# Kernel optimization log

Hardware: AMD Instinct MI355X
Metric: run time of the kernel (lower is better)

Reference implementation:

```python
import jax, jax.numpy as jnp
import numpy as np

D_MODEL = 1024
D_STATE = 16
DT_RANK = 64  # d_model // 16 ('auto')
DT_MIN = 0.001
DT_MAX = 0.1


def setup_inputs() -> dict:
    key = jax.random.key(0)
    ks = jax.random.split(key, 7)
    B, S = 2, 2048
    return {
        "x": jax.random.normal(ks[0], (B, S, D_MODEL), jnp.float32),
        "w_in": jax.random.normal(ks[1], (D_MODEL, D_MODEL), jnp.float32) / np.sqrt(D_MODEL).astype(np.float32),
        "w_x": jax.random.normal(ks[2], (D_MODEL, DT_RANK + 2 * D_STATE), jnp.float32) / np.sqrt(D_MODEL).astype(np.float32),
        "w_dt": jax.random.normal(ks[3], (DT_RANK, D_MODEL), jnp.float32) / np.sqrt(DT_RANK).astype(np.float32),
        "b_dt": jnp.zeros((D_MODEL,), jnp.float32),
        "A_log": jax.random.normal(ks[5], (D_MODEL, D_STATE), jnp.float32) * 0.5,
        "Dp": jax.random.normal(ks[6], (D_MODEL,), jnp.float32),
    }


def reference(x, w_in, w_x, w_dt, b_dt, A_log, Dp):
    # x: (b, s, d)
    x_in = jnp.einsum('bsd,de->bse', x, w_in)          # in_proj, (b,s,d_inner=d)
    proj = jnp.einsum('bsd,dp->bsp', x_in, w_x)        # x_proj, (b,s,dt_rank+2n)
    dt_low, Bm, Cm = jnp.split(proj, [DT_RANK, DT_RANK + D_STATE], axis=-1)
    # dt_proj + softplus + range scaling -> (b,s,d)
    dt = jax.nn.softplus(jnp.einsum('bsr,rd->bsd', dt_low, w_dt) + b_dt) * (DT_MAX - DT_MIN) + DT_MIN
    A = -jnp.exp(A_log)                                # (d, n), strictly negative

    b, s, d = x.shape
    h0 = jnp.zeros((b, d, D_STATE), x.dtype)

    # time-major streams for scan
    dt_tm = jnp.swapaxes(dt, 0, 1)     # (s,b,d)
    u_tm = jnp.swapaxes(x_in, 0, 1)    # (s,b,d)
    B_tm = jnp.swapaxes(Bm, 0, 1)      # (s,b,n)
    C_tm = jnp.swapaxes(Cm, 0, 1)      # (s,b,n)

    def step(h, inp):
        dtt, ut, bt, ct = inp
        dA = dtt[:, :, None] * A                      # (b,d,n) = dt[b,d]*A[d,n]
        barA = jnp.exp(dA)
        # bar_B = dA; source sums the input term over channel dim d (keepdim)
        inp_term = jnp.einsum('bdn,bn,bd->bn', dA, bt, ut)  # (b,n)
        h = barA * h + inp_term[:, None, :]           # broadcast over d
        y = jnp.einsum('bdn,bn->bd', h, ct) + Dp * ut # (b,d)
        return h, y

    _, ys = jax.lax.scan(step, h0, (dt_tm, u_tm, B_tm, C_tm))  # ys: (s,b,d)
    return jnp.swapaxes(ys, 0, 1)                     # (b,s,d)
```

## Files before the change

kernel.cpp:

```cpp
#include <hip/hip_runtime.h>
#include <hip/hip_bf16.h>

#define D_MODEL 1024
#define D_STATE 16
#define DT_RANK 64
#define SEQ 2048
#define BATCH 2
#define M_TOTAL 4096
#define CHUNKS 64
#define CLEN 32
#define LOG2E 1.44269504088896f

typedef __bf16 bf16x8 __attribute__((ext_vector_type(8)));
typedef float f32x4 __attribute__((ext_vector_type(4)));

__device__ __forceinline__ unsigned short f2bf(float f) {
    union { float f; unsigned int u; } v; v.f = f;
    unsigned int r = v.u + 0x7FFFu + ((v.u >> 16) & 1u);
    return (unsigned short)(r >> 16);
}
__device__ __forceinline__ float bf2f(unsigned short u) {
    union { unsigned int i; float f; } v; v.i = ((unsigned int)u) << 16; return v.f;
}
__device__ __forceinline__ void gload16(const void* g, void* l) {
    __builtin_amdgcn_global_load_lds(
        (const __attribute__((address_space(1))) unsigned int*)g,
        (__attribute__((address_space(3))) unsigned int*)l, 16, 0, 0);
}
__device__ __forceinline__ float fexp2(float x) { return __builtin_amdgcn_exp2f(x); }

__global__ void __launch_bounds__(256) k_setup(const float* __restrict__ x,
                                               const float* __restrict__ win,
                                               const float* __restrict__ wx,
                                               const float* __restrict__ wdt,
                                               const float* __restrict__ alog,
                                               unsigned short* __restrict__ xb,
                                               unsigned short* __restrict__ bt,
                                               unsigned short* __restrict__ wxT,
                                               unsigned short* __restrict__ wxBC,
                                               unsigned short* __restrict__ wdtT,
                                               float* __restrict__ aneg,
                                               unsigned short* __restrict__ anegT) {
    __shared__ float tile[32][33];
    int blk = blockIdx.x;
    int t = threadIdx.x;
    if (blk < 4096) {
        int i = blk * 256 + t;
        float4 v = reinterpret_cast<const float4*>(x)[i];
        ushort4 o;
        o.x = f2bf(v.x); o.y = f2bf(v.y); o.z = f2bf(v.z); o.w = f2bf(v.w);
        reinterpret_cast<ushort4*>(xb)[i] = o;
    } else if (blk < 5120) {
        int blk2 = blk - 4096;
        int bx = blk2 & 31, by = blk2 >> 5;
        int tx = t & 31, ty = t >> 5;
        int xc = bx * 32 + tx;
#pragma unroll
        for (int j = 0; j < 4; j++)
            tile[ty + 8 * j][tx] = win[(by * 32 + ty + 8 * j) * D_MODEL + xc];
        __syncthreads();
        int x2 = by * 32 + tx;
#pragma unroll
        for (int j = 0; j < 4; j++)
            bt[(bx * 32 + ty + 8 * j) * D_MODEL + x2] = f2bf(tile[tx][ty + 8 * j]);
    } else if (blk < 5376) {
        int idx = (blk - 5120) * 256 + t;
        int e = idx & 1023, p = idx >> 10;
        wxT[p * D_MODEL + e] = f2bf(wx[e * 96 + p]);
    } else if (blk < 5504) {
        int idx = (blk - 5376) * 256 + t;
        int e = idx & 1023, p = idx >> 10;
        wxBC[p * D_MODEL + e] = f2bf(wx[e * 96 + 64 + p]);
    } else if (blk < 5568) {
        int i = (blk - 5504) * 256 + t;
        float v = -expf(alog[i]);
        aneg[i] = v * LOG2E;
        anegT[(i & 15) * D_MODEL + (i >> 4)] = f2bf(v);
    } else {
        int idx = (blk - 5568) * 256 + t;
        int d = idx & 1023, k = idx >> 10;
        wdtT[d * DT_RANK + k] = f2bf(wdt[k * D_MODEL + d]);
    }
}

__global__ void __launch_bounds__(256) k_gemm_xin(const unsigned short* __restrict__ xb,
                                                  const unsigned short* __restrict__ bt,
                                                  unsigned short* __restrict__ xinb) {
    __shared__ unsigned short sA[2][64 * 64];
    __shared__ unsigned short sB[2][128 * 64];
    int bid = blockIdx.x;
    int m0 = (bid & 63) * 64;
    int n0 = (bid >> 6) * 128;
    int t = threadIdx.x;
    int lane = t & 63;
    int w = t >> 6;
    int wm = (w >> 1) * 32, wn = (w & 1) * 64;
    int c = lane & 15, q = lane >> 4;

    const unsigned short* gA[2];
    const unsigned short* gB[4];
#pragma unroll
    for (int L = 0; L < 2; L++) {
        int s = L * 256 + t;
        int row = s >> 3, ch = (s & 7) ^ (row & 7);
        gA[L] = xb + (m0 + row) * D_MODEL + ch * 8;
    }
#pragma unroll
    for (int L = 0; L < 4; L++) {
        int s = L * 256 + t;
        int row = s >> 3, ch = (s & 7) ^ (row & 7);
        gB[L] = bt + (n0 + row) * D_MODEL + ch * 8;
    }

    f32x4 acc[2][4] = {};
    {
        char* la = (char*)&sA[0][0] + w * 1024;
        char* lb = (char*)&sB[0][0] + w * 1024;
#pragma unroll
        for (int L = 0; L < 2; L++) gload16(gA[L], la + L * 4096);
#pragma unroll
        for (int L = 0; L < 4; L++) gload16(gB[L], lb + L * 4096);
    }
    int cur = 0;
    for (int it = 0; it < 16; it++) {
        __syncthreads();
        if (it + 1 < 16) {
            int kn = (it + 1) * 64;
            char* la = (char*)&sA[cur ^ 1][0] + w * 1024;
            char* lb = (char*)&sB[cur ^ 1][0] + w * 1024;
#pragma unroll
            for (int L = 0; L < 2; L++) gload16(gA[L] + kn, la + L * 4096);
#pragma unroll
            for (int L = 0; L < 4; L++) gload16(gB[L] + kn, lb + L * 4096);
        }
#pragma unroll
        for (int kk = 0; kk < 2; kk++) {
            int perm = (((kk << 2) | q) ^ (c & 7)) << 3;
            bf16x8 af[2], bfr[4];
#pragma unroll
            for (int i = 0; i < 2; i++)
                af[i] = *reinterpret_cast<const bf16x8*>(&sA[cur][(wm + i * 16 + c) * 64 + perm]);
#pragma unroll
            for (int j = 0; j < 4; j++)
                bfr[j] = *reinterpret_cast<const bf16x8*>(&sB[cur][(wn + j * 16 + c) * 64 + perm]);
#pragma unroll
            for (int i = 0; i < 2; i++)
#pragma unroll
                for (int j = 0; j < 4; j++)
                    acc[i][j] = __builtin_amdgcn_mfma_f32_16x16x32_bf16(bfr[j], af[i], acc[i][j], 0, 0, 0);
        }
        cur ^= 1;
    }
#pragma unroll
    for (int i = 0; i < 2; i++) {
        int row = m0 + wm + i * 16 + c;
#pragma unroll
        for (int j = 0; j < 4; j++) {
            int col = n0 + wn + j * 16 + q * 4;
            ushort4 o;
            o.x = f2bf(acc[i][j][0]); o.y = f2bf(acc[i][j][1]);
            o.z = f2bf(acc[i][j][2]); o.w = f2bf(acc[i][j][3]);
            *reinterpret_cast<ushort4*>(&xinb[row * D_MODEL + col]) = o;
        }
    }
}

__global__ void __launch_bounds__(256) k_xlow(const unsigned short* __restrict__ xinb,
                                              const unsigned short* __restrict__ wxT,
                                              unsigned short* __restrict__ xlow) {
    int m0 = blockIdx.x * 64;
    int t = threadIdx.x;
    int lane = t & 63, w = t >> 6;
    int c = lane & 15, q = lane >> 4;
    int row = m0 + w * 16 + c;
    f32x4 acc[4] = {};
    const unsigned short* pa = xinb + row * D_MODEL + q * 8;
    const unsigned short* pw = wxT + c * D_MODEL + q * 8;
#pragma unroll 4
    for (int k0 = 0; k0 < D_MODEL; k0 += 32) {
        bf16x8 a0 = *reinterpret_cast<const bf16x8*>(pa + k0);
#pragma unroll
        for (int j = 0; j < 4; j++) {
            bf16x8 wf = *reinterpret_cast<const bf16x8*>(pw + j * 16 * D_MODEL + k0);
            acc[j] = __builtin_amdgcn_mfma_f32_16x16x32_bf16(wf, a0, acc[j], 0, 0, 0);
        }
    }
#pragma unroll
    for (int j = 0; j < 4; j++) {
        ushort4 o;
        o.x = f2bf(acc[j][0]); o.y = f2bf(acc[j][1]);
        o.z = f2bf(acc[j][2]); o.w = f2bf(acc[j][3]);
        *reinterpret_cast<ushort4*>(&xlow[row * DT_RANK + j * 16 + q * 4]) = o;
    }
}

__global__ void __launch_bounds__(256) k_gemm_dt(const unsigned short* __restrict__ xlow,
                                                 const unsigned short* __restrict__ wdtT,
                                                 const float* __restrict__ bdt,
                                                 unsigned short* __restrict__ dtb) {
    __shared__ unsigned short sA[128 * 64];
    int bid = blockIdx.x;
    int m0 = (bid & 31) * 128;
    int n0 = (bid >> 5) * 128;
    int t = threadIdx.x;
    int lane = t & 63, w = t >> 6;
    int c = lane & 15, q = lane >> 4;

    {
        char* la = (char*)&sA[0] + w * 1024;
#pragma unroll
        for (int L = 0; L < 4; L++) {
            int s = L * 256 + t;
            int row = s >> 3, ch = (s & 7) ^ (row & 7);
            gload16(xlow + (m0 + row) * DT_RANK + ch * 8, la + L * 4096);
        }
    }
    __syncthreads();

    int mw = m0 + w * 32;
    f32x4 acc[2][8] = {};
#pragma unroll
    for (int kk = 0; kk < 2; kk++) {
        bf16x8 af[2];
#pragma unroll
        for (int i = 0; i < 2; i++)
            af[i] = *reinterpret_cast<const bf16x8*>(
                &sA[(w * 32 + i * 16 + c) * 64 + ((((kk << 2) | q)) ^ (c & 7)) * 8]);
#pragma unroll
        for (int j = 0; j < 8; j++) {
            bf16x8 bfr = *reinterpret_cast<const bf16x8*>(
                &wdtT[(n0 + j * 16 + c) * DT_RANK + kk * 32 + q * 8]);
            acc[0][j] = __builtin_amdgcn_mfma_f32_16x16x32_bf16(bfr, af[0], acc[0][j], 0, 0, 0);
            acc[1][j] = __builtin_amdgcn_mfma_f32_16x16x32_bf16(bfr, af[1], acc[1][j], 0, 0, 0);
        }
    }
#pragma unroll
    for (int i = 0; i < 2; i++) {
        int row = mw + i * 16 + c;
#pragma unroll
        for (int j = 0; j < 8; j++) {
            int dcol = n0 + j * 16 + q * 4;
            float4 bv = *reinterpret_cast<const float4*>(&bdt[dcol]);
            ushort4 o;
            {
                float xv = acc[i][j][0] + bv.x;
                float sp = fmaxf(xv, 0.f) + __logf(1.f + __expf(-fabsf(xv)));
                o.x = f2bf(sp * 0.099f + 0.001f);
            }
            {
                float xv = acc[i][j][1] + bv.y;
                float sp = fmaxf(xv, 0.f) + __logf(1.f + __expf(-fabsf(xv)));
                o.y = f2bf(sp * 0.099f + 0.001f);
            }
            {
                float xv = acc[i][j][2] + bv.z;
                float sp = fmaxf(xv, 0.f) + __logf(1.f + __expf(-fabsf(xv)));
                o.z = f2bf(sp * 0.099f + 0.001f);
            }
            {
                float xv = acc[i][j][3] + bv.w;
                float sp = fmaxf(xv, 0.f) + __logf(1.f + __expf(-fabsf(xv)));
                o.w = f2bf(sp * 0.099f + 0.001f);
            }
            *reinterpret_cast<ushort4*>(&dtb[row * D_MODEL + dcol]) = o;
        }
    }
}

__global__ void __launch_bounds__(256) k_bcw(const unsigned short* __restrict__ xinb,
                                             const unsigned short* __restrict__ dtb,
                                             const unsigned short* __restrict__ wxBC,
                                             const unsigned short* __restrict__ anegT,
                                             float* __restrict__ bcp,
                                             float* __restrict__ wpp) {
    int bid = blockIdx.x;
    int m0 = (bid & 31) * 128;
    int ks = bid >> 5;
    int kbase = ks * 128;
    int t = threadIdx.x;
    int lane = t & 63, w = t >> 6;
    int c = lane & 15, q = lane >> 4;
    int mw = m0 + w * 32;
    f32x4 accb[2][2] = {};
    f32x4 accw[2] = {};
    const unsigned short* pa0 = xinb + (mw + c) * D_MODEL + kbase + q * 8;
    const unsigned short* pa1 = pa0 + 16 * D_MODEL;
    const unsigned short* pt0 = dtb + (mw + c) * D_MODEL + kbase + q * 8;
    const unsigned short* pt1 = pt0 + 16 * D_MODEL;
    const unsigned short* pb0 = wxBC + c * D_MODEL + kbase + q * 8;
    const unsigned short* pb1 = pb0 + 16 * D_MODEL;
    const unsigned short* pA = anegT + c * D_MODEL + kbase + q * 8;
#pragma unroll
    for (int k0 = 0; k0 < 128; k0 += 32) {
        bf16x8 a0 = *reinterpret_cast<const bf16x8*>(pa0 + k0);
        bf16x8 a1 = *reinterpret_cast<const bf16x8*>(pa1 + k0);
        bf16x8 t0 = *reinterpret_cast<const bf16x8*>(pt0 + k0);
        bf16x8 t1 = *reinterpret_cast<const bf16x8*>(pt1 + k0);
        bf16x8 b0 = *reinterpret_cast<const bf16x8*>(pb0 + k0);
        bf16x8 b1 = *reinterpret_cast<const bf16x8*>(pb1 + k0);
        bf16x8 bA = *reinterpret_cast<const bf16x8*>(pA + k0);
        bf16x8 g0, g1;
#pragma unroll
        for (int e = 0; e < 8; e++) {
            g0[e] = (__bf16)((float)t0[e] * (float)a0[e]);
            g1[e] = (__bf16)((float)t1[e] * (float)a1[e]);
        }
        accb[0][0] = __builtin_amdgcn_mfma_f32_16x16x32_bf16(b0, a0, accb[0][0], 0, 0, 0);
        accb[0][1] = __builtin_amdgcn_mfma_f32_16x16x32_bf16(b1, a0, accb[0][1], 0, 0, 0);
        accb[1][0] = __builtin_amdgcn_mfma_f32_16x16x32_bf16(b0, a1, accb[1][0], 0, 0, 0);
        accb[1][1] = __builtin_amdgcn_mfma_f32_16x16x32_bf16(b1, a1, accb[1][1], 0, 0, 0);
        accw[0] = __builtin_amdgcn_mfma_f32_16x16x32_bf16(bA, g0, accw[0], 0, 0, 0);
        accw[1] = __builtin_amdgcn_mfma_f32_16x16x32_bf16(bA, g1, accw[1], 0, 0, 0);
    }
#pragma unroll
    for (int i = 0; i < 2; i++) {
        int row = mw + i * 16 + c;
#pragma unroll
        for (int j = 0; j < 2; j++)
            *reinterpret_cast<f32x4*>(&bcp[(ks * M_TOTAL + row) * 32 + j * 16 + q * 4]) = accb[i][j];
        *reinterpret_cast<f32x4*>(&wpp[(ks * M_TOTAL + row) * 16 + q * 4]) = accw[i];
    }
}

__global__ void __launch_bounds__(256) k_scan1(const unsigned short* __restrict__ dtb,
                                               const float* __restrict__ bcp,
                                               const float* __restrict__ wpp,
                                               const float* __restrict__ aneg,
                                               float* __restrict__ h_loc,
                                               float* __restrict__ dtsum) {
    __shared__ unsigned short s_dt[16][256];
    __shared__ float s_w[16][16];
    int dc = blockIdx.x & 3;
    int c = (blockIdx.x >> 2) & (CHUNKS - 1);
    int b = blockIdx.x >> 8;
    int tid = threadIdx.x;
    int d = dc * 256 + tid;
    float Ad[16];
    const float4* ar = reinterpret_cast<const float4*>(aneg + d * 16);
#pragma unroll
    for (int j = 0; j < 4; j++) {
        float4 a4 = ar[j];
        Ad[4 * j + 0] = a4.x; Ad[4 * j + 1] = a4.y;
        Ad[4 * j + 2] = a4.z; Ad[4 * j + 3] = a4.w;
    }
    float h[16];
#pragma unroll
    for (int n = 0; n < 16; n++) h[n] = 0.f;
    float dts = 0.f;

    int r8 = tid >> 5, col8 = (tid & 31) * 8;
    for (int t0 = 0; t0 < CLEN; t0 += 16) {
        __syncthreads();
        int rowbase = b * SEQ + c * CLEN + t0;
        *reinterpret_cast<uint4*>(&s_dt[r8][col8]) =
            *reinterpret_cast<const uint4*>(dtb + (rowbase + r8) * D_MODEL + dc * 256 + col8);
        *reinterpret_cast<uint4*>(&s_dt[8 + r8][col8]) =
            *reinterpret_cast<const uint4*>(dtb + (rowbase + 8 + r8) * D_MODEL + dc * 256 + col8);
        {
            int r = tid >> 4, n = tid & 15;
            int row = rowbase + r;
            float sB = 0.f, sw = 0.f;
#pragma unroll
            for (int ks = 0; ks < 8; ks++) {
                sB += bcp[(ks * M_TOTAL + row) * 32 + n];
                sw += wpp[(ks * M_TOTAL + row) * 16 + n];
            }
            s_w[r][n] = sB * sw;
        }
        __syncthreads();
        for (int r = 0; r < 16; r++) {
            float dtv = bf2f(s_dt[r][tid]);
            dts += dtv;
#pragma unroll
            for (int n = 0; n < 16; n++) {
                float ba = fexp2(dtv * Ad[n]);
                h[n] = fmaf(ba, h[n], s_w[r][n]);
            }
        }
    }
    int base = ((b * CHUNKS + c) * D_MODEL + d) * 16;
#pragma unroll
    for (int j = 0; j < 4; j++) {
        f32x4 v = {h[4 * j], h[4 * j + 1], h[4 * j + 2], h[4 * j + 3]};
        *reinterpret_cast<f32x4*>(h_loc + base + 4 * j) = v;
    }
    dtsum[(b * CHUNKS + c) * D_MODEL + d] = dts;
}

__global__ void __launch_bounds__(128) k_scan2(float* __restrict__ h_inout,
                                               const float* __restrict__ dtsum,
                                               const float* __restrict__ aneg) {
    int idx = blockIdx.x * 128 + threadIdx.x;
    int n = idx & 15;
    int d = (idx >> 4) & (D_MODEL - 1);
    int b = idx >> 14;
    float A = aneg[d * 16 + n];
    float H = 0.f;
    int off0 = b * CHUNKS * D_MODEL + d;
#pragma unroll 1
    for (int g = 0; g < CHUNKS; g += 8) {
        float hl[8], ds[8];
#pragma unroll
        for (int j = 0; j < 8; j++) {
            int off = off0 + (g + j) * D_MODEL;
            hl[j] = h_inout[off * 16 + n];
            ds[j] = dtsum[off];
        }
#pragma unroll
        for (int j = 0; j < 8; j++) {
            int off = off0 + (g + j) * D_MODEL;
            float P = fexp2(ds[j] * A);
            h_inout[off * 16 + n] = H;
            H = fmaf(P, H, hl[j]);
        }
    }
}

__global__ void __launch_bounds__(256) k_scan3(const unsigned short* __restrict__ dtb,
                                               const unsigned short* __restrict__ xinb,
                                               const float* __restrict__ bcp,
                                               const float* __restrict__ wpp,
                                               const float* __restrict__ aneg,
                                               const float* __restrict__ dp,
                                               const float* __restrict__ H_in,
                                               float* __restrict__ out) {
    __shared__ unsigned short s_dt[16][256], s_u[16][256];
    __shared__ float s_w[16][16], s_c[16][16];
    int dc = blockIdx.x & 3;
    int c = (blockIdx.x >> 2) & (CHUNKS - 1);
    int b = blockIdx.x >> 8;
    int tid = threadIdx.x;
    int d = dc * 256 + tid;
    float Ad[16];
    const float4* ar = reinterpret_cast<const float4*>(aneg + d * 16);
#pragma unroll
    for (int j = 0; j < 4; j++) {
        float4 a4 = ar[j];
        Ad[4 * j + 0] = a4.x; Ad[4 * j + 1] = a4.y;
        Ad[4 * j + 2] = a4.z; Ad[4 * j + 3] = a4.w;
    }
    float Dpd = dp[d];
    float h[16];
    int base = ((b * CHUNKS + c) * D_MODEL + d) * 16;
#pragma unroll
    for (int j = 0; j < 4; j++) {
        f32x4 v = *reinterpret_cast<const f32x4*>(H_in + base + 4 * j);
        h[4 * j] = v[0]; h[4 * j + 1] = v[1]; h[4 * j + 2] = v[2]; h[4 * j + 3] = v[3];
    }

    int r8 = tid >> 5, col8 = (tid & 31) * 8;
    for (int t0 = 0; t0 < CLEN; t0 += 16) {
        __syncthreads();
        int rowbase = b * SEQ + c * CLEN + t0;
        *reinterpret_cast<uint4*>(&s_dt[r8][col8]) =
            *reinterpret_cast<const uint4*>(dtb + (rowbase + r8) * D_MODEL + dc * 256 + col8);
        *reinterpret_cast<uint4*>(&s_dt[8 + r8][col8]) =
            *reinterpret_cast<const uint4*>(dtb + (rowbase + 8 + r8) * D_MODEL + dc * 256 + col8);
        *reinterpret_cast<uint4*>(&s_u[r8][col8]) =
            *reinterpret_cast<const uint4*>(xinb + (rowbase + r8) * D_MODEL + dc * 256 + col8);
        *reinterpret_cast<uint4*>(&s_u[8 + r8][col8]) =
            *reinterpret_cast<const uint4*>(xinb + (rowbase + 8 + r8) * D_MODEL + dc * 256 + col8);
        {
            int r = tid >> 4, n = tid & 15;
            int row = rowbase + r;
            float sB = 0.f, sw = 0.f, sC = 0.f;
#pragma unroll
            for (int ks = 0; ks < 8; ks++) {
                sB += bcp[(ks * M_TOTAL + row) * 32 + n];
                sC += bcp[(ks * M_TOTAL + row) * 32 + 16 + n];
                sw += wpp[(ks * M_TOTAL + row) * 16 + n];
            }
            s_w[r][n] = sB * sw;
            s_c[r][n] = sC;
        }
        __syncthreads();
        for (int r = 0; r < 16; r++) {
            float dtv = bf2f(s_dt[r][tid]), uv = bf2f(s_u[r][tid]);
            float y = Dpd * uv;
#pragma unroll
            for (int n = 0; n < 16; n++) {
                float ba = fexp2(dtv * Ad[n]);
                h[n] = fmaf(ba, h[n], s_w[r][n]);
                y = fmaf(h[n], s_c[r][n], y);
            }
            out[(rowbase + r) * D_MODEL + d] = y;
        }
    }
}

extern "C" void kernel_launch(void* const* d_in, const int* in_sizes, int n_in,
                              void* d_out, int out_size, void* d_ws, size_t ws_size,
                              hipStream_t stream) {
    const float* x     = (const float*)d_in[0];
    const float* w_in  = (const float*)d_in[1];
    const float* w_x   = (const float*)d_in[2];
    const float* w_dt  = (const float*)d_in[3];
    const float* b_dt  = (const float*)d_in[4];
    const float* A_log = (const float*)d_in[5];
    const float* Dp    = (const float*)d_in[6];
    float* out = (float*)d_out;

    char* ws = (char*)d_ws;
    unsigned short* xb   = (unsigned short*)(ws + 0);
    unsigned short* bt   = (unsigned short*)(ws + 8388608);
    unsigned short* xinb = (unsigned short*)(ws + 10485760);
    unsigned short* dtb  = (unsigned short*)(ws + 18874368);
    float* bcp           = (float*)(ws + 27262976);
    float* wpp           = (float*)(ws + 31457280);
    unsigned short* xlow = (unsigned short*)(ws + 33554432);
    unsigned short* wxT  = (unsigned short*)(ws + 35651584);
    unsigned short* wxBC = (unsigned short*)(ws + 35782656);
    unsigned short* wdtT = (unsigned short*)(ws + 35848192);
    float* aneg          = (float*)(ws + 35979264);
    unsigned short* anegT= (unsigned short*)(ws + 36044800);
    float* h_loc         = (float*)(ws + 0);
    float* dtsum         = (float*)(ws + 8388608);

    k_setup<<<5824, 256, 0, stream>>>(x, w_in, w_x, w_dt, A_log, xb, bt, wxT, wxBC, wdtT, aneg, anegT);
    k_gemm_xin<<<512, 256, 0, stream>>>(xb, bt, xinb);
    k_xlow<<<64, 256, 0, stream>>>(xinb, wxT, xlow);
    k_gemm_dt<<<256, 256, 0, stream>>>(xlow, wdtT, b_dt, dtb);
    k_bcw<<<256, 256, 0, stream>>>(xinb, dtb, wxBC, anegT, bcp, wpp);
    k_scan1<<<BATCH * CHUNKS * 4, 256, 0, stream>>>(dtb, bcp, wpp, aneg, h_loc, dtsum);
    k_scan2<<<256, 128, 0, stream>>>(h_loc, dtsum, aneg);
    k_scan3<<<BATCH * CHUNKS * 4, 256, 0, stream>>>(dtb, xinb, bcp, wpp, aneg, Dp, h_loc, out);
}
```

Measured before the change: 175.8 us.

## Fuse BC projection and three scan phases into one cooperative kernel

Replaces the k_bcw, k_scan1, k_scan2 and k_scan3 launches with a single cooperative kernel of 256 blocks of 512 threads. Each block runs two logical 256-thread sub-blocks, and the phases are separated by grid.sync() instead of kernel boundaries. The aim is to remove launch gaps and tail effects between the four small kernels. In exchange it adds grid-wide barrier cost, fixes occupancy at one large block per CU, and requires cooperative launch support.

```diff
diff --git a/kernel.cpp b/kernel.cpp
--- a/kernel.cpp
+++ b/kernel.cpp
@@ -1,5 +1,8 @@
 #include <hip/hip_runtime.h>
 #include <hip/hip_bf16.h>
+#include <hip/hip_cooperative_groups.h>
+
+namespace cg = cooperative_groups;
 
 #define D_MODEL 1024
 #define D_STATE 16
@@ -267,223 +270,206 @@
     }
 }
 
-__global__ void __launch_bounds__(256) k_bcw(const unsigned short* __restrict__ xinb,
-                                             const unsigned short* __restrict__ dtb,
-                                             const unsigned short* __restrict__ wxBC,
-                                             const unsigned short* __restrict__ anegT,
-                                             float* __restrict__ bcp,
-                                             float* __restrict__ wpp) {
-    int bid = blockIdx.x;
-    int m0 = (bid & 31) * 128;
-    int ks = bid >> 5;
-    int kbase = ks * 128;
-    int t = threadIdx.x;
-    int lane = t & 63, w = t >> 6;
-    int c = lane & 15, q = lane >> 4;
-    int mw = m0 + w * 32;
-    f32x4 accb[2][2] = {};
-    f32x4 accw[2] = {};
-    const unsigned short* pa0 = xinb + (mw + c) * D_MODEL + kbase + q * 8;
-    const unsigned short* pa1 = pa0 + 16 * D_MODEL;
-    const unsigned short* pt0 = dtb + (mw + c) * D_MODEL + kbase + q * 8;
-    const unsigned short* pt1 = pt0 + 16 * D_MODEL;
-    const unsigned short* pb0 = wxBC + c * D_MODEL + kbase + q * 8;
-    const unsigned short* pb1 = pb0 + 16 * D_MODEL;
-    const unsigned short* pA = anegT + c * D_MODEL + kbase + q * 8;
-#pragma unroll
-    for (int k0 = 0; k0 < 128; k0 += 32) {
-        bf16x8 a0 = *reinterpret_cast<const bf16x8*>(pa0 + k0);
-        bf16x8 a1 = *reinterpret_cast<const bf16x8*>(pa1 + k0);
-        bf16x8 t0 = *reinterpret_cast<const bf16x8*>(pt0 + k0);
-        bf16x8 t1 = *reinterpret_cast<const bf16x8*>(pt1 + k0);
-        bf16x8 b0 = *reinterpret_cast<const bf16x8*>(pb0 + k0);
-        bf16x8 b1 = *reinterpret_cast<const bf16x8*>(pb1 + k0);
-        bf16x8 bA = *reinterpret_cast<const bf16x8*>(pA + k0);
-        bf16x8 g0, g1;
-#pragma unroll
-        for (int e = 0; e < 8; e++) {
-            g0[e] = (__bf16)((float)t0[e] * (float)a0[e]);
-            g1[e] = (__bf16)((float)t1[e] * (float)a1[e]);
-        }
-        accb[0][0] = __builtin_amdgcn_mfma_f32_16x16x32_bf16(b0, a0, accb[0][0], 0, 0, 0);
-        accb[0][1] = __builtin_amdgcn_mfma_f32_16x16x32_bf16(b1, a0, accb[0][1], 0, 0, 0);
-        accb[1][0] = __builtin_amdgcn_mfma_f32_16x16x32_bf16(b0, a1, accb[1][0], 0, 0, 0);
-        accb[1][1] = __builtin_amdgcn_mfma_f32_16x16x32_bf16(b1, a1, accb[1][1], 0, 0, 0);
-        accw[0] = __builtin_amdgcn_mfma_f32_16x16x32_bf16(bA, g0, accw[0], 0, 0, 0);
-        accw[1] = __builtin_amdgcn_mfma_f32_16x16x32_bf16(bA, g1, accw[1], 0, 0, 0);
-    }
-#pragma unroll
-    for (int i = 0; i < 2; i++) {
-        int row = mw + i * 16 + c;
+__global__ void __launch_bounds__(512) k_tail(const unsigned short* __restrict__ dtb,
+                                              const unsigned short* __restrict__ xinb,
+                                              const unsigned short* __restrict__ wxBC,
+                                              const unsigned short* __restrict__ anegT,
+                                              const float* __restrict__ aneg,
+                                              const float* __restrict__ dp,
+                                              float* __restrict__ bcp,
+                                              float* __restrict__ wpp,
+                                              float* __restrict__ h_loc,
+                                              float* __restrict__ dtsum,
+                                              float* __restrict__ out) {
+    cg::grid_group grid = cg::this_grid();
+    __shared__ unsigned short s_dt[2][16][256];
+    __shared__ unsigned short s_u[2][16][256];
+    __shared__ float s_w[2][16][16];
+    __shared__ float s_c[2][16][16];
+
+    int tid = threadIdx.x;
+    int half = tid >> 8;
+    int lt = tid & 255;
+    int ob = blockIdx.x * 2 + half;
+    int lane = lt & 63;
+    int c16 = lane & 15, q = lane >> 4;
+
+    {
+        int m0 = (ob & 63) * 64;
+        int ks = ob >> 6;
+        int kbase = ks * 128;
+        int w2 = lt >> 6;
+        int mw = m0 + w2 * 16;
+        f32x4 accb[2] = {};
+        f32x4 accw = {};
+        const unsigned short* pa = xinb + (mw + c16) * D_MODEL + kbase + q * 8;
+        const unsigned short* pt = dtb + (mw + c16) * D_MODEL + kbase + q * 8;
+        const unsigned short* pb0 = wxBC + c16 * D_MODEL + kbase + q * 8;
+        const unsigned short* pb1 = pb0 + 16 * D_MODEL;
+        const unsigned short* pA = anegT + c16 * D_MODEL + kbase + q * 8;
+#pragma unroll
+        for (int k0 = 0; k0 < 128; k0 += 32) {
+            bf16x8 a0 = *reinterpret_cast<const bf16x8*>(pa + k0);
+            bf16x8 t0 = *reinterpret_cast<const bf16x8*>(pt + k0);
+            bf16x8 b0 = *reinterpret_cast<const bf16x8*>(pb0 + k0);
+            bf16x8 b1 = *reinterpret_cast<const bf16x8*>(pb1 + k0);
+            bf16x8 bA = *reinterpret_cast<const bf16x8*>(pA + k0);
+            bf16x8 g0;
+#pragma unroll
+            for (int e = 0; e < 8; e++) g0[e] = (__bf16)((float)t0[e] * (float)a0[e]);
+            accb[0] = __builtin_amdgcn_mfma_f32_16x16x32_bf16(b0, a0, accb[0], 0, 0, 0);
+            accb[1] = __builtin_amdgcn_mfma_f32_16x16x32_bf16(b1, a0, accb[1], 0, 0, 0);
+            accw = __builtin_amdgcn_mfma_f32_16x16x32_bf16(bA, g0, accw, 0, 0, 0);
+        }
+        int row = mw + c16;
 #pragma unroll
         for (int j = 0; j < 2; j++)
-            *reinterpret_cast<f32x4*>(&bcp[(ks * M_TOTAL + row) * 32 + j * 16 + q * 4]) = accb[i][j];
-        *reinterpret_cast<f32x4*>(&wpp[(ks * M_TOTAL + row) * 16 + q * 4]) = accw[i];
-    }
-}
-
-__global__ void __launch_bounds__(256) k_scan1(const unsigned short* __restrict__ dtb,
-                                               const float* __restrict__ bcp,
-                                               const float* __restrict__ wpp,
-                                               const float* __restrict__ aneg,
-                                               float* __restrict__ h_loc,
-                                               float* __restrict__ dtsum) {
-    __shared__ unsigned short s_dt[16][256];
-    __shared__ float s_w[16][16];
-    int dc = blockIdx.x & 3;
-    int c = (blockIdx.x >> 2) & (CHUNKS - 1);
-    int b = blockIdx.x >> 8;
-    int tid = threadIdx.x;
-    int d = dc * 256 + tid;
-    float Ad[16];
-    const float4* ar = reinterpret_cast<const float4*>(aneg + d * 16);
-#pragma unroll
-    for (int j = 0; j < 4; j++) {
-        float4 a4 = ar[j];
-        Ad[4 * j + 0] = a4.x; Ad[4 * j + 1] = a4.y;
-        Ad[4 * j + 2] = a4.z; Ad[4 * j + 3] = a4.w;
-    }
-    float h[16];
-#pragma unroll
-    for (int n = 0; n < 16; n++) h[n] = 0.f;
-    float dts = 0.f;
-
-    int r8 = tid >> 5, col8 = (tid & 31) * 8;
-    for (int t0 = 0; t0 < CLEN; t0 += 16) {
-        __syncthreads();
-        int rowbase = b * SEQ + c * CLEN + t0;
-        *reinterpret_cast<uint4*>(&s_dt[r8][col8]) =
-            *reinterpret_cast<const uint4*>(dtb + (rowbase + r8) * D_MODEL + dc * 256 + col8);
-        *reinterpret_cast<uint4*>(&s_dt[8 + r8][col8]) =
-            *reinterpret_cast<const uint4*>(dtb + (rowbase + 8 + r8) * D_MODEL + dc * 256 + col8);
-        {
-            int r = tid >> 4, n = tid & 15;
-            int row = rowbase + r;
-            float sB = 0.f, sw = 0.f;
-#pragma unroll
-            for (int ks = 0; ks < 8; ks++) {
-                sB += bcp[(ks * M_TOTAL + row) * 32 + n];
-                sw += wpp[(ks * M_TOTAL + row) * 16 + n];
-            }
-            s_w[r][n] = sB * sw;
-        }
-        __syncthreads();
-        for (int r = 0; r < 16; r++) {
-            float dtv = bf2f(s_dt[r][tid]);
-            dts += dtv;
-#pragma unroll
-            for (int n = 0; n < 16; n++) {
-                float ba = fexp2(dtv * Ad[n]);
-                h[n] = fmaf(ba, h[n], s_w[r][n]);
-            }
-        }
-    }
-    int base = ((b * CHUNKS + c) * D_MODEL + d) * 16;
-#pragma unroll
-    for (int j = 0; j < 4; j++) {
-        f32x4 v = {h[4 * j], h[4 * j + 1], h[4 * j + 2], h[4 * j + 3]};
-        *reinterpret_cast<f32x4*>(h_loc + base + 4 * j) = v;
-    }
-    dtsum[(b * CHUNKS + c) * D_MODEL + d] = dts;
-}
-
-__global__ void __launch_bounds__(128) k_scan2(float* __restrict__ h_inout,
-                                               const float* __restrict__ dtsum,
-                                               const float* __restrict__ aneg) {
-    int idx = blockIdx.x * 128 + threadIdx.x;
-    int n = idx & 15;
-    int d = (idx >> 4) & (D_MODEL - 1);
-    int b = idx >> 14;
-    float A = aneg[d * 16 + n];
-    float H = 0.f;
-    int off0 = b * CHUNKS * D_MODEL + d;
+            *reinterpret_cast<f32x4*>(&bcp[(ks * M_TOTAL + row) * 32 + j * 16 + q * 4]) = accb[j];
+        *reinterpret_cast<f32x4*>(&wpp[(ks * M_TOTAL + row) * 16 + q * 4]) = accw;
+    }
+    grid.sync();
+
+    int dc = ob & 3;
+    int cch = (ob >> 2) & (CHUNKS - 1);
+    int bb = ob >> 8;
+    int d = dc * 256 + lt;
+    int r8 = lt >> 5, col8 = (lt & 31) * 8;
+
+    {
+        float Ad[16];
+        const float4* ar = reinterpret_cast<const float4*>(aneg + d * 16);
+#pragma unroll
+        for (int j = 0; j < 4; j++) {
+            float4 a4 = ar[j];
+            Ad[4 * j + 0] = a4.x; Ad[4 * j + 1] = a4.y;
+            Ad[4 * j + 2] = a4.z; Ad[4 * j + 3] = a4.w;
+        }
+        float h[16];
+#pragma unroll
+        for (int n = 0; n < 16; n++) h[n] = 0.f;
+        float dts = 0.f;
+        for (int t0 = 0; t0 < CLEN; t0 += 16) {
+            __syncthreads();
+            int rowbase = bb * SEQ + cch * CLEN + t0;
+            *reinterpret_cast<uint4*>(&s_dt[half][r8][col8]) =
+                *reinterpret_cast<const uint4*>(dtb + (rowbase + r8) * D_MODEL + dc * 256 + col8);
+            *reinterpret_cast<uint4*>(&s_dt[half][8 + r8][col8]) =
+                *reinterpret_cast<const uint4*>(dtb + (rowbase + 8 + r8) * D_MODEL + dc * 256 + col8);
+            {
+                int r = lt >> 4, n = lt & 15;
+                int row = rowbase + r;
+                float sB = 0.f, sw = 0.f;
+#pragma unroll
+                for (int ks = 0; ks < 8; ks++) {
+                    sB += bcp[(ks * M_TOTAL + row) * 32 + n];
+                    sw += wpp[(ks * M_TOTAL + row) * 16 + n];
+                }
+                s_w[half][r][n] = sB * sw;
+            }
+            __syncthreads();
+            for (int r = 0; r < 16; r++) {
+                float dtv = bf2f(s_dt[half][r][lt]);
+                dts += dtv;
+#pragma unroll
+                for (int n = 0; n < 16; n++) {
+                    float ba = fexp2(dtv * Ad[n]);
+                    h[n] = fmaf(ba, h[n], s_w[half][r][n]);
+                }
+            }
+        }
+        int base = ((bb * CHUNKS + cch) * D_MODEL + d) * 16;
+#pragma unroll
+        for (int j = 0; j < 4; j++) {
+            f32x4 v = {h[4 * j], h[4 * j + 1], h[4 * j + 2], h[4 * j + 3]};
+            *reinterpret_cast<f32x4*>(h_loc + base + 4 * j) = v;
+        }
+        dtsum[(bb * CHUNKS + cch) * D_MODEL + d] = dts;
+    }
+    grid.sync();
+
+    {
+        int idx = blockIdx.x * 512 + tid;
+        if (idx < 32768) {
+            int n = idx & 15;
+            int dd = (idx >> 4) & (D_MODEL - 1);
+            int b2 = idx >> 14;
+            float A = aneg[dd * 16 + n];
+            float H = 0.f;
+            int off0 = b2 * CHUNKS * D_MODEL + dd;
 #pragma unroll 1
-    for (int g = 0; g < CHUNKS; g += 8) {
-        float hl[8], ds[8];
-#pragma unroll
-        for (int j = 0; j < 8; j++) {
-            int off = off0 + (g + j) * D_MODEL;
-            hl[j] = h_inout[off * 16 + n];
-            ds[j] = dtsum[off];
-        }
-#pragma unroll
-        for (int j = 0; j < 8; j++) {
-            int off = off0 + (g + j) * D_MODEL;
-            float P = fexp2(ds[j] * A);
-            h_inout[off * 16 + n] = H;
-            H = fmaf(P, H, hl[j]);
-        }
-    }
-}
-
-__global__ void __launch_bounds__(256) k_scan3(const unsigned short* __restrict__ dtb,
-                                               const unsigned short* __restrict__ xinb,
-                                               const float* __restrict__ bcp,
-                                               const float* __restrict__ wpp,
-                                               const float* __restrict__ aneg,
-                                               const float* __restrict__ dp,
-                                               const float* __restrict__ H_in,
-                                               float* __restrict__ out) {
-    __shared__ unsigned short s_dt[16][256], s_u[16][256];
-    __shared__ float s_w[16][16], s_c[16][16];
-    int dc = blockIdx.x & 3;
-    int c = (blockIdx.x >> 2) & (CHUNKS - 1);
-    int b = blockIdx.x >> 8;
-    int tid = threadIdx.x;
-    int d = dc * 256 + tid;
-    float Ad[16];
-    const float4* ar = reinterpret_cast<const float4*>(aneg + d * 16);
-#pragma unroll
-    for (int j = 0; j < 4; j++) {
-        float4 a4 = ar[j];
-        Ad[4 * j + 0] = a4.x; Ad[4 * j + 1] = a4.y;
-        Ad[4 * j + 2] = a4.z; Ad[4 * j + 3] = a4.w;
-    }
-    float Dpd = dp[d];
-    float h[16];
-    int base = ((b * CHUNKS + c) * D_MODEL + d) * 16;
-#pragma unroll
-    for (int j = 0; j < 4; j++) {
-        f32x4 v = *reinterpret_cast<const f32x4*>(H_in + base + 4 * j);
-        h[4 * j] = v[0]; h[4 * j + 1] = v[1]; h[4 * j + 2] = v[2]; h[4 * j + 3] = v[3];
-    }
-
-    int r8 = tid >> 5, col8 = (tid & 31) * 8;
-    for (int t0 = 0; t0 < CLEN; t0 += 16) {
-        __syncthreads();
-        int rowbase = b * SEQ + c * CLEN + t0;
-        *reinterpret_cast<uint4*>(&s_dt[r8][col8]) =
-            *reinterpret_cast<const uint4*>(dtb + (rowbase + r8) * D_MODEL + dc * 256 + col8);
-        *reinterpret_cast<uint4*>(&s_dt[8 + r8][col8]) =
-            *reinterpret_cast<const uint4*>(dtb + (rowbase + 8 + r8) * D_MODEL + dc * 256 + col8);
-        *reinterpret_cast<uint4*>(&s_u[r8][col8]) =
-            *reinterpret_cast<const uint4*>(xinb + (rowbase + r8) * D_MODEL + dc * 256 + col8);
-        *reinterpret_cast<uint4*>(&s_u[8 + r8][col8]) =
-            *reinterpret_cast<const uint4*>(xinb + (rowbase + 8 + r8) * D_MODEL + dc * 256 + col8);
-        {
-            int r = tid >> 4, n = tid & 15;
-            int row = rowbase + r;
-            float sB = 0.f, sw = 0.f, sC = 0.f;
-#pragma unroll
-            for (int ks = 0; ks < 8; ks++) {
-                sB += bcp[(ks * M_TOTAL + row) * 32 + n];
-                sC += bcp[(ks * M_TOTAL + row) * 32 + 16 + n];
-                sw += wpp[(ks * M_TOTAL + row) * 16 + n];
-            }
-            s_w[r][n] = sB * sw;
-            s_c[r][n] = sC;
-        }
-        __syncthreads();
-        for (int r = 0; r < 16; r++) {
-            float dtv = bf2f(s_dt[r][tid]), uv = bf2f(s_u[r][tid]);
-            float y = Dpd * uv;
-#pragma unroll
-            for (int n = 0; n < 16; n++) {
-                float ba = fexp2(dtv * Ad[n]);
-                h[n] = fmaf(ba, h[n], s_w[r][n]);
-                y = fmaf(h[n], s_c[r][n], y);
-            }
-            out[(rowbase + r) * D_MODEL + d] = y;
+            for (int g = 0; g < CHUNKS; g += 8) {
+                float hl[8], ds[8];
+#pragma unroll
+                for (int j = 0; j < 8; j++) {
+                    int off = off0 + (g + j) * D_MODEL;
+                    hl[j] = h_loc[off * 16 + n];
+                    ds[j] = dtsum[off];
+                }
+#pragma unroll
+                for (int j = 0; j < 8; j++) {
+                    int off = off0 + (g + j) * D_MODEL;
+                    float P = fexp2(ds[j] * A);
+                    h_loc[off * 16 + n] = H;
+                    H = fmaf(P, H, hl[j]);
+                }
+            }
+        }
+    }
+    grid.sync();
+
+    {
+        float Ad[16];
+        const float4* ar = reinterpret_cast<const float4*>(aneg + d * 16);
+#pragma unroll
+        for (int j = 0; j < 4; j++) {
+            float4 a4 = ar[j];
+            Ad[4 * j + 0] = a4.x; Ad[4 * j + 1] = a4.y;
+            Ad[4 * j + 2] = a4.z; Ad[4 * j + 3] = a4.w;
+        }
+        float Dpd = dp[d];
+        float h[16];
+        int base = ((bb * CHUNKS + cch) * D_MODEL + d) * 16;
+#pragma unroll
+        for (int j = 0; j < 4; j++) {
+            f32x4 v = *reinterpret_cast<const f32x4*>(h_loc + base + 4 * j);
+            h[4 * j] = v[0]; h[4 * j + 1] = v[1]; h[4 * j + 2] = v[2]; h[4 * j + 3] = v[3];
+        }
+        for (int t0 = 0; t0 < CLEN; t0 += 16) {
+            __syncthreads();
+            int rowbase = bb * SEQ + cch * CLEN + t0;
+            *reinterpret_cast<uint4*>(&s_dt[half][r8][col8]) =
+                *reinterpret_cast<const uint4*>(dtb + (rowbase + r8) * D_MODEL + dc * 256 + col8);
+            *reinterpret_cast<uint4*>(&s_dt[half][8 + r8][col8]) =
+                *reinterpret_cast<const uint4*>(dtb + (rowbase + 8 + r8) * D_MODEL + dc * 256 + col8);
+            *reinterpret_cast<uint4*>(&s_u[half][r8][col8]) =
+                *reinterpret_cast<const uint4*>(xinb + (rowbase + r8) * D_MODEL + dc * 256 + col8);
+            *reinterpret_cast<uint4*>(&s_u[half][8 + r8][col8]) =
+                *reinterpret_cast<const uint4*>(xinb + (rowbase + 8 + r8) * D_MODEL + dc * 256 + col8);
+            {
+                int r = lt >> 4, n = lt & 15;
+                int row = rowbase + r;
+                float sB = 0.f, sw = 0.f, sC = 0.f;
+#pragma unroll
+                for (int ks = 0; ks < 8; ks++) {
+                    sB += bcp[(ks * M_TOTAL + row) * 32 + n];
+                    sC += bcp[(ks * M_TOTAL + row) * 32 + 16 + n];
+                    sw += wpp[(ks * M_TOTAL + row) * 16 + n];
+                }
+                s_w[half][r][n] = sB * sw;
+                s_c[half][r][n] = sC;
+            }
+            __syncthreads();
+            for (int r = 0; r < 16; r++) {
+                float dtv = bf2f(s_dt[half][r][lt]), uv = bf2f(s_u[half][r][lt]);
+                float y = Dpd * uv;
+#pragma unroll
+                for (int n = 0; n < 16; n++) {
+                    float ba = fexp2(dtv * Ad[n]);
+                    h[n] = fmaf(ba, h[n], s_w[half][r][n]);
+                    y = fmaf(h[n], s_c[half][r][n], y);
+                }
+                out[(rowbase + r) * D_MODEL + d] = y;
+            }
         }
     }
 }
@@ -520,8 +506,19 @@
     k_gemm_xin<<<512, 256, 0, stream>>>(xb, bt, xinb);
     k_xlow<<<64, 256, 0, stream>>>(xinb, wxT, xlow);
     k_gemm_dt<<<256, 256, 0, stream>>>(xlow, wdtT, b_dt, dtb);
-    k_bcw<<<256, 256, 0, stream>>>(xinb, dtb, wxBC, anegT, bcp, wpp);
-    k_scan1<<<BATCH * CHUNKS * 4, 256, 0, stream>>>(dtb, bcp, wpp, aneg, h_loc, dtsum);
-    k_scan2<<<256, 128, 0, stream>>>(h_loc, dtsum, aneg);
-    k_scan3<<<BATCH * CHUNKS * 4, 256, 0, stream>>>(dtb, xinb, bcp, wpp, aneg, Dp, h_loc, out);
-}
+    {
+        const unsigned short* a0 = dtb;
+        const unsigned short* a1 = xinb;
+        const unsigned short* a2 = wxBC;
+        const unsigned short* a3 = anegT;
+        const float* a4 = aneg;
+        const float* a5 = Dp;
+        float* a6 = bcp;
+        float* a7 = wpp;
+        float* a8 = h_loc;
+        float* a9 = dtsum;
+        float* a10 = out;
+        void* args[] = {&a0, &a1, &a2, &a3, &a4, &a5, &a6, &a7, &a8, &a9, &a10};
+        hipLaunchCooperativeKernel((const void*)k_tail, dim3(256), dim3(512), args, 0, stream);
+    }
+}
```

After: 275.8 us. 1.57x slower.

## Fuse x_proj dt_low GEMM with dt_proj softplus into one kernel

Applied to the files above, without the earlier changes.

Merges the k_xlow and k_gemm_dt kernels into a single k_dt kernel. The dt_low tile is now staged in swizzled shared memory instead of a global round-trip. Each block then loops over all 1024 output columns, applying bias, softplus and scaling before writing dt. This removes one launch and the xlow global write and read. In exchange, the dt GEMM and softplus run on only 64 blocks instead of 256, which lowers parallelism on a large GPU.

```diff
diff --git a/kernel.cpp b/kernel.cpp
--- a/kernel.cpp
+++ b/kernel.cpp
@@ -165,14 +165,19 @@
     }
 }
 
-__global__ void __launch_bounds__(256) k_xlow(const unsigned short* __restrict__ xinb,
-                                              const unsigned short* __restrict__ wxT,
-                                              unsigned short* __restrict__ xlow) {
+__global__ void __launch_bounds__(256) k_dt(const unsigned short* __restrict__ xinb,
+                                            const unsigned short* __restrict__ wxT,
+                                            const unsigned short* __restrict__ wdtT,
+                                            const float* __restrict__ bdt,
+                                            unsigned short* __restrict__ dtb) {
+    __shared__ unsigned short sX[64 * 64];
     int m0 = blockIdx.x * 64;
     int t = threadIdx.x;
     int lane = t & 63, w = t >> 6;
     int c = lane & 15, q = lane >> 4;
-    int row = m0 + w * 16 + c;
+    int lrow = w * 16 + c;
+    int row = m0 + lrow;
+
     f32x4 acc[4] = {};
     const unsigned short* pa = xinb + row * D_MODEL + q * 8;
     const unsigned short* pw = wxT + c * D_MODEL + q * 8;
@@ -187,83 +192,56 @@
     }
 #pragma unroll
     for (int j = 0; j < 4; j++) {
+        int col = j * 16 + q * 4;
+        int chunk = col >> 3, within = col & 7;
+        int swz = chunk ^ (lrow & 7);
         ushort4 o;
         o.x = f2bf(acc[j][0]); o.y = f2bf(acc[j][1]);
         o.z = f2bf(acc[j][2]); o.w = f2bf(acc[j][3]);
-        *reinterpret_cast<ushort4*>(&xlow[row * DT_RANK + j * 16 + q * 4]) = o;
-    }
-}
-
-__global__ void __launch_bounds__(256) k_gemm_dt(const unsigned short* __restrict__ xlow,
-                                                 const unsigned short* __restrict__ wdtT,
-                                                 const float* __restrict__ bdt,
-                                                 unsigned short* __restrict__ dtb) {
-    __shared__ unsigned short sA[128 * 64];
-    int bid = blockIdx.x;
-    int m0 = (bid & 31) * 128;
-    int n0 = (bid >> 5) * 128;
-    int t = threadIdx.x;
-    int lane = t & 63, w = t >> 6;
-    int c = lane & 15, q = lane >> 4;
-
-    {
-        char* la = (char*)&sA[0] + w * 1024;
-#pragma unroll
-        for (int L = 0; L < 4; L++) {
-            int s = L * 256 + t;
-            int row = s >> 3, ch = (s & 7) ^ (row & 7);
-            gload16(xlow + (m0 + row) * DT_RANK + ch * 8, la + L * 4096);
-        }
+        *reinterpret_cast<ushort4*>(&sX[lrow * 64 + swz * 8 + within]) = o;
     }
     __syncthreads();
 
-    int mw = m0 + w * 32;
-    f32x4 acc[2][8] = {};
+    bf16x8 af[2];
 #pragma unroll
     for (int kk = 0; kk < 2; kk++) {
-        bf16x8 af[2];
-#pragma unroll
-        for (int i = 0; i < 2; i++)
-            af[i] = *reinterpret_cast<const bf16x8*>(
-                &sA[(w * 32 + i * 16 + c) * 64 + ((((kk << 2) | q)) ^ (c & 7)) * 8]);
-#pragma unroll
-        for (int j = 0; j < 8; j++) {
+        int chunk = kk * 4 + q;
+        int swz = chunk ^ (lrow & 7);
+        af[kk] = *reinterpret_cast<const bf16x8*>(&sX[lrow * 64 + swz * 8]);
+    }
+#pragma unroll 4
+    for (int j = 0; j < 64; j++) {
+        f32x4 a = {};
+#pragma unroll
+        for (int kk = 0; kk < 2; kk++) {
             bf16x8 bfr = *reinterpret_cast<const bf16x8*>(
-                &wdtT[(n0 + j * 16 + c) * DT_RANK + kk * 32 + q * 8]);
-            acc[0][j] = __builtin_amdgcn_mfma_f32_16x16x32_bf16(bfr, af[0], acc[0][j], 0, 0, 0);
-            acc[1][j] = __builtin_amdgcn_mfma_f32_16x16x32_bf16(bfr, af[1], acc[1][j], 0, 0, 0);
-        }
-    }
-#pragma unroll
-    for (int i = 0; i < 2; i++) {
-        int row = mw + i * 16 + c;
-#pragma unroll
-        for (int j = 0; j < 8; j++) {
-            int dcol = n0 + j * 16 + q * 4;
-            float4 bv = *reinterpret_cast<const float4*>(&bdt[dcol]);
-            ushort4 o;
-            {
-                float xv = acc[i][j][0] + bv.x;
-                float sp = fmaxf(xv, 0.f) + __logf(1.f + __expf(-fabsf(xv)));
-                o.x = f2bf(sp * 0.099f + 0.001f);
-            }
-            {
-                float xv = acc[i][j][1] + bv.y;
-                float sp = fmaxf(xv, 0.f) + __logf(1.f + __expf(-fabsf(xv)));
-                o.y = f2bf(sp * 0.099f + 0.001f);
-            }
-            {
-                float xv = acc[i][j][2] + bv.z;
-                float sp = fmaxf(xv, 0.f) + __logf(1.f + __expf(-fabsf(xv)));
-                o.z = f2bf(sp * 0.099f + 0.001f);
-            }
-            {
-                float xv = acc[i][j][3] + bv.w;
-                float sp = fmaxf(xv, 0.f) + __logf(1.f + __expf(-fabsf(xv)));
-                o.w = f2bf(sp * 0.099f + 0.001f);
-            }
-            *reinterpret_cast<ushort4*>(&dtb[row * D_MODEL + dcol]) = o;
-        }
+                &wdtT[(j * 16 + c) * DT_RANK + kk * 32 + q * 8]);
+            a = __builtin_amdgcn_mfma_f32_16x16x32_bf16(bfr, af[kk], a, 0, 0, 0);
+        }
+        int dcol = j * 16 + q * 4;
+        float4 bv = *reinterpret_cast<const float4*>(&bdt[dcol]);
+        ushort4 o;
+        {
+            float xv = a[0] + bv.x;
+            float sp = fmaxf(xv, 0.f) + __logf(1.f + __expf(-fabsf(xv)));
+            o.x = f2bf(sp * 0.099f + 0.001f);
+        }
+        {
+            float xv = a[1] + bv.y;
+            float sp = fmaxf(xv, 0.f) + __logf(1.f + __expf(-fabsf(xv)));
+            o.y = f2bf(sp * 0.099f + 0.001f);
+        }
+        {
+            float xv = a[2] + bv.z;
+            float sp = fmaxf(xv, 0.f) + __logf(1.f + __expf(-fabsf(xv)));
+            o.z = f2bf(sp * 0.099f + 0.001f);
+        }
+        {
+            float xv = a[3] + bv.w;
+            float sp = fmaxf(xv, 0.f) + __logf(1.f + __expf(-fabsf(xv)));
+            o.w = f2bf(sp * 0.099f + 0.001f);
+        }
+        *reinterpret_cast<ushort4*>(&dtb[row * D_MODEL + dcol]) = o;
     }
 }
 
@@ -507,7 +485,6 @@
     unsigned short* dtb  = (unsigned short*)(ws + 18874368);
     float* bcp           = (float*)(ws + 27262976);
     float* wpp           = (float*)(ws + 31457280);
-    unsigned short* xlow = (unsigned short*)(ws + 33554432);
     unsigned short* wxT  = (unsigned short*)(ws + 35651584);
     unsigned short* wxBC = (unsigned short*)(ws + 35782656);
     unsigned short* wdtT = (unsigned short*)(ws + 35848192);
@@ -518,8 +495,7 @@
 
     k_setup<<<5824, 256, 0, stream>>>(x, w_in, w_x, w_dt, A_log, xb, bt, wxT, wxBC, wdtT, aneg, anegT);
     k_gemm_xin<<<512, 256, 0, stream>>>(xb, bt, xinb);
-    k_xlow<<<64, 256, 0, stream>>>(xinb, wxT, xlow);
-    k_gemm_dt<<<256, 256, 0, stream>>>(xlow, wdtT, b_dt, dtb);
+    k_dt<<<64, 256, 0, stream>>>(xinb, wxT, wdtT, b_dt, dtb);
     k_bcw<<<256, 256, 0, stream>>>(xinb, dtb, wxBC, anegT, bcp, wpp);
     k_scan1<<<BATCH * CHUNKS * 4, 256, 0, stream>>>(dtb, bcp, wpp, aneg, h_loc, dtsum);
     k_scan2<<<256, 128, 0, stream>>>(h_loc, dtsum, aneg);
```

Result: slower. 204.0 us (+16.1%).
